# Performance work log

Measured on AMD Instinct MI355X. Metric: run time of the kernel, lower is better.

## Reference

```python
import jax, jax.numpy as jnp
import numpy as np
import math

KEY_SIZE = 128  # init arg; scale = 1/sqrt(key_size)


def setup_inputs() -> dict:
    key = jax.random.key(0)
    kq, kk, kv = jax.random.split(key, 3)
    B, LQ, LK, D, DV = 16, 2048, 2048, 128, 128
    q = jax.random.normal(kq, (B, LQ, D), dtype=jnp.float32)
    k = jax.random.normal(kk, (B, LK, D), dtype=jnp.float32)
    v = jax.random.normal(kv, (B, LK, DV), dtype=jnp.float32)
    return {"q": q, "k": k, "v": v}


def reference(q, k, v):
    scale = 1.0 / math.sqrt(KEY_SIZE)
    # scores: [B, Lq, Lk]
    scores = jnp.einsum('bqd,bkd->bqk', q, k) * scale
    probs = jax.nn.softmax(scores, axis=-1)
    # dropout with p=0.0 is identity (eval-equivalent)
    return jnp.einsum('bqk,bkv->bqv', probs, v)
```

## Files before the change

### kernel.cpp

```cpp
#include <hip/hip_runtime.h>
#include <hip/hip_bf16.h>

typedef float f32x4 __attribute__((ext_vector_type(4)));
typedef float f32x16 __attribute__((ext_vector_type(16)));
typedef short bf16x8 __attribute__((ext_vector_type(8)));
typedef unsigned u32x4 __attribute__((ext_vector_type(4)));

constexpr int NB = 16, LQ = 2048, LK = 2048, D = 128, DV = 128;
constexpr int NTH = 32;
constexpr float SCALE = 0.08838834764831843f;
constexpr float LOG2E = 1.4426950408889634f;
constexpr float QSCALE = SCALE * LOG2E;
constexpr float SHIFT = 12.0f;

__device__ __forceinline__ unsigned short f2bfs(float f) {
  __hip_bfloat16 h = __float2bfloat16(f);
  return __builtin_bit_cast(unsigned short, h);
}

__device__ __forceinline__ unsigned short f2bf(float f) {
  unsigned int u = __float_as_uint(f);
  u += 0x7FFFu + ((u >> 16) & 1u);
  return (unsigned short)(u >> 16);
}

__device__ __forceinline__ int swz2(int row) {
  return (row ^ (row >> 1) ^ (row >> 3)) & 7;
}

__device__ __forceinline__ int swap23(int m) {
  return (m & ~12) | ((m & 4) << 1) | ((m & 8) >> 1);
}

typedef const __attribute__((address_space(1))) void* gas1_t;
typedef __attribute__((address_space(3))) void* las3_t;
__device__ __forceinline__ void gload16(const void* g, void* l) {
  __builtin_amdgcn_global_load_lds((gas1_t)g, (las3_t)l, 16, 0, 0);
}

__device__ __forceinline__ unsigned pk2(float lo, float hi) {
  unsigned short a = f2bfs(lo), b = f2bfs(hi);
  return (unsigned)a | ((unsigned)b << 16);
}

__device__ __forceinline__ void mk_pb(const f32x16& s, bf16x8& pe, bf16x8& po) {
  u32x4 e = {pk2(s[0], s[1]), pk2(s[2], s[3]), pk2(s[4], s[5]), pk2(s[6], s[7])};
  pe = __builtin_bit_cast(bf16x8, e);
  u32x4 od = {pk2(s[8], s[9]), pk2(s[10], s[11]), pk2(s[12], s[13]), pk2(s[14], s[15])};
  po = __builtin_bit_cast(bf16x8, od);
}

__global__ __launch_bounds__(256) void conv_k2(const float* __restrict__ kp,
                                               unsigned short* __restrict__ out) {
  __shared__ __align__(16) unsigned short tk[4096];
  const int T = blockIdx.x, b = blockIdx.y;
  const int tid = threadIdx.x;
  const int k = tid >> 3, cc = tid & 7, d0 = cc * 16;
  const float* src = kp + ((long)(b * LK) + 32 * T + k) * D + d0;
  f32x4 a0 = ((const f32x4*)src)[0];
  f32x4 a1 = ((const f32x4*)src)[1];
  f32x4 a2 = ((const f32x4*)src)[2];
  f32x4 a3 = ((const f32x4*)src)[3];
  bf16x8 r0, r1;
  #pragma unroll
  for (int j = 0; j < 4; ++j) {
    r0[j] = (short)f2bfs(a0[j]); r0[4 + j] = (short)f2bfs(a1[j]);
    r1[j] = (short)f2bfs(a2[j]); r1[4 + j] = (short)f2bfs(a3[j]);
  }
  const int rr = swap23(k);
  *(bf16x8*)&tk[(2 * cc) * 256 + rr * 8] = r0;
  *(bf16x8*)&tk[(2 * cc + 1) * 256 + rr * 8] = r1;
  __syncthreads();
  unsigned short* dst = out + ((long)(b * 64 + T)) * 4096 + tid * 16;
  *(bf16x8*)dst = *(const bf16x8*)&tk[tid * 16];
  *(bf16x8*)(dst + 8) = *(const bf16x8*)&tk[tid * 16 + 8];
}

__global__ __launch_bounds__(256) void conv_v2(const float* __restrict__ vp,
                                               unsigned short* __restrict__ out) {
  __shared__ __align__(16) unsigned short tv[4096];
  const int T = blockIdx.x, b = blockIdx.y;
  const int tid = threadIdx.x;
  const int k = tid >> 3, cc = tid & 7, d0 = cc * 16;
  const float* src = vp + ((long)(b * LK) + 32 * T + k) * DV + d0;
  f32x4 a0 = ((const f32x4*)src)[0];
  f32x4 a1 = ((const f32x4*)src)[1];
  f32x4 a2 = ((const f32x4*)src)[2];
  f32x4 a3 = ((const f32x4*)src)[3];
  unsigned short vals[16];
  #pragma unroll
  for (int j = 0; j < 4; ++j) {
    vals[j]      = f2bfs(a0[j]);
    vals[4 + j]  = f2bfs(a1[j]);
    vals[8 + j]  = f2bfs(a2[j]);
    vals[12 + j] = f2bfs(a3[j]);
  }
  const int vbase = (k >> 3) * 1024 + (k & 7);
  #pragma unroll
  for (int i = 0; i < 16; ++i)
    tv[vbase + (d0 + i) * 8] = vals[i];
  __syncthreads();
  unsigned short* dst = out + ((long)(b * 64 + T)) * 4096 + tid * 16;
  *(bf16x8*)dst = *(const bf16x8*)&tv[tid * 16];
  *(bf16x8*)(dst + 8) = *(const bf16x8*)&tv[tid * 16 + 8];
}

__global__ __launch_bounds__(128, 2) void attn_fwd13(
    const float* __restrict__ qp, const unsigned short* __restrict__ wsK2,
    const unsigned short* __restrict__ wsV2, float* __restrict__ op) {
  __shared__ __align__(16) unsigned short sm[16384];

  const int tid = threadIdx.x;
  const int wid = tid >> 6;
  const int lane = tid & 63;
  const int q32 = lane & 31;
  const int hi  = lane >> 5;

  const int bid = blockIdx.x;
  const int sbid = (bid & 7) * 128 + (bid >> 3);
  const int b = sbid >> 6;
  const int qb = (sbid & 63) * 32;

  bf16x8 aq[8];
  {
    const float* qrow = qp + ((long)(b * LQ + qb + q32)) * D + hi * 8;
    #pragma unroll
    for (int st = 0; st < 8; ++st) {
      f32x4 x0 = *(const f32x4*)(qrow + st * 16);
      f32x4 x1 = *(const f32x4*)(qrow + st * 16 + 4);
      #pragma unroll
      for (int j = 0; j < 4; ++j) {
        aq[st][j]     = (short)f2bfs(x0[j] * QSCALE);
        aq[st][4 + j] = (short)f2bfs(x1[j] * QSCALE);
      }
    }
  }
  __builtin_amdgcn_sched_barrier(0);

  const int lbase = wid * 8192;
  const unsigned short* kps = wsK2 + ((long)(b * 64 + wid * 32)) * 4096;
  const unsigned short* vgb = wsV2 + ((long)(b * 64 + wid * 32)) * 4096
                              + hi * 1024 + q32 * 8;

  auto stageK = [&](int buf, int t) {
    const long toff = (long)t * 4096;
    const int lb = lbase + buf * 4096;
    #pragma unroll
    for (int it = 0; it < 8; ++it) {
      const int ci = it * 64 + lane;
      gload16(kps + toff + ci * 8, &sm[lb + ci * 8]);
    }
  };

  stageK(0, 0);
  stageK(1, 1);

  f32x16 o[4];
  #pragma unroll
  for (int mt = 0; mt < 4; ++mt) o[mt] = (f32x16){};
  float l_s = 0.f;

  const int kub = lbase + hi * 256 + q32 * 8;

  f32x16 sA, sB;
  bf16x8 vfA[8], vfB[8];

  asm volatile("s_waitcnt vmcnt(8)" ::: "memory");
  __builtin_amdgcn_sched_barrier(0);
  #pragma unroll
  for (int i = 0; i < 16; ++i) sA[i] = -SHIFT;
  #pragma unroll
  for (int st = 0; st < 8; ++st) {
    bf16x8 k0 = *(const bf16x8*)&sm[kub + st * 512];
    sA = __builtin_amdgcn_mfma_f32_32x32x16_bf16(k0, aq[st], sA, 0, 0, 0);
  }
  #pragma unroll
  for (int ks = 0; ks < 2; ++ks)
    #pragma unroll
    for (int mt = 0; mt < 4; ++mt)
      vfA[ks * 4 + mt] = *(const bf16x8*)(vgb + ks * 2048 + mt * 256);
  asm volatile("s_waitcnt lgkmcnt(0)" ::: "memory");
  __builtin_amdgcn_sched_barrier(0);
  stageK(0, 2);

  auto body = [&](int t, f32x16& s_prev, f32x16& s_next,
                  bf16x8 (&v_prev)[8], bf16x8 (&v_next)[8]) {
    if (t < NTH - 1) {
      asm volatile("s_waitcnt vmcnt(8)" ::: "memory");
    } else {
      asm volatile("s_waitcnt vmcnt(0)" ::: "memory");
    }
    __builtin_amdgcn_sched_barrier(0);

    const int kb = kub + (t & 1) * 4096;

    #pragma unroll
    for (int i = 0; i < 16; ++i) s_next[i] = -SHIFT;
    __builtin_amdgcn_s_setprio(1);
    #pragma unroll
    for (int st = 0; st < 8; ++st) {
      bf16x8 k0 = *(const bf16x8*)&sm[kb + st * 512];
      s_next = __builtin_amdgcn_mfma_f32_32x32x16_bf16(k0, aq[st], s_next, 0, 0, 0);
    }
    __builtin_amdgcn_s_setprio(0);

    const unsigned short* vt = vgb + (long)t * 4096;
    #pragma unroll
    for (int ks = 0; ks < 2; ++ks)
      #pragma unroll
      for (int mt = 0; mt < 4; ++mt)
        v_next[ks * 4 + mt] = *(const bf16x8*)(vt + ks * 2048 + mt * 256);

    #pragma unroll
    for (int i = 0; i < 16; ++i) s_prev[i] = exp2f(s_prev[i]);
    float s8[8];
    #pragma unroll
    for (int i = 0; i < 8; ++i) s8[i] = s_prev[i] + s_prev[i + 8];
    float sum = ((s8[0] + s8[1]) + (s8[2] + s8[3])) +
                ((s8[4] + s8[5]) + (s8[6] + s8[7]));
    l_s += sum + __shfl_xor(sum, 32);
    bf16x8 pb0, pb1;
    mk_pb(s_prev, pb0, pb1);

    __builtin_amdgcn_s_setprio(1);
    #pragma unroll
    for (int mt = 0; mt < 4; ++mt)
      o[mt] = __builtin_amdgcn_mfma_f32_32x32x16_bf16(v_prev[mt], pb0, o[mt], 0, 0, 0);
    #pragma unroll
    for (int mt = 0; mt < 4; ++mt)
      o[mt] = __builtin_amdgcn_mfma_f32_32x32x16_bf16(v_prev[4 + mt], pb1, o[mt], 0, 0, 0);
    __builtin_amdgcn_s_setprio(0);

    asm volatile("s_waitcnt lgkmcnt(0)" ::: "memory");
    __builtin_amdgcn_sched_barrier(0);
    if (t + 2 < NTH) stageK(t & 1, t + 2);
  };

  for (int tt = 1; tt < NTH - 1; tt += 2) {
    body(tt,     sA, sB, vfA, vfB);
    body(tt + 1, sB, sA, vfB, vfA);
  }
  body(NTH - 1, sA, sB, vfA, vfB);

  {
    asm volatile("s_waitcnt vmcnt(0)" ::: "memory");
    __builtin_amdgcn_sched_barrier(0);
    #pragma unroll
    for (int i = 0; i < 16; ++i) sB[i] = exp2f(sB[i]);
    float s8[8];
    #pragma unroll
    for (int i = 0; i < 8; ++i) s8[i] = sB[i] + sB[i + 8];
    float sum = ((s8[0] + s8[1]) + (s8[2] + s8[3])) +
                ((s8[4] + s8[5]) + (s8[6] + s8[7]));
    l_s += sum + __shfl_xor(sum, 32);
    bf16x8 pb0, pb1;
    mk_pb(sB, pb0, pb1);
    #pragma unroll
    for (int mt = 0; mt < 4; ++mt)
      o[mt] = __builtin_amdgcn_mfma_f32_32x32x16_bf16(vfB[mt], pb0, o[mt], 0, 0, 0);
    #pragma unroll
    for (int mt = 0; mt < 4; ++mt)
      o[mt] = __builtin_amdgcn_mfma_f32_32x32x16_bf16(vfB[4 + mt], pb1, o[mt], 0, 0, 0);
  }

  float* wreg = (float*)sm;
  __syncthreads();
  if (wid == 1) {
    #pragma unroll
    for (int j4 = 0; j4 < 16; ++j4) {
      const int mt = j4 >> 2, a = j4 & 3;
      f32x4 v = {o[mt][4 * a], o[mt][4 * a + 1], o[mt][4 * a + 2], o[mt][4 * a + 3]};
      *(f32x4*)&wreg[lane * 64 + ((j4 ^ (lane & 15)) << 2)] = v;
    }
    wreg[4096 + lane] = l_s;
  }
  __syncthreads();
  if (wid == 0) {
    const float l1 = wreg[4096 + lane];
    const float inv = 1.f / (l_s + l1);
    float* dst = op + ((long)(b * LQ + qb + q32)) * DV;
    #pragma unroll
    for (int j4 = 0; j4 < 16; ++j4) {
      const int mt = j4 >> 2, a = j4 & 3;
      f32x4 pv = *(const f32x4*)&wreg[lane * 64 + ((j4 ^ (lane & 15)) << 2)];
      f32x4 r;
      #pragma unroll
      for (int i = 0; i < 4; ++i) r[i] = (o[mt][4 * a + i] + pv[i]) * inv;
      *(f32x4*)&dst[32 * mt + 8 * a + 4 * hi] = r;
    }
  }
}

__device__ __forceinline__ int swzc(int row, int c16) {
  return c16 ^ ((row ^ (row >> 3)) & 7);
}

__global__ __launch_bounds__(256, 2) void attn_fwd(
    const float* __restrict__ qp, const float* __restrict__ kp,
    const float* __restrict__ vp, float* __restrict__ op) {
  __shared__ __align__(16) unsigned short smm[28672];
  const int tid = threadIdx.x, wid = tid >> 6, lane = tid & 63;
  const int g = lane >> 4, c = lane & 15;
  const int b = blockIdx.y, qb = blockIdx.x * 64;
  const float* qg = qp + ((long)b * LQ + qb) * D;
  const float* kg = kp + (long)b * LK * D;
  const float* vg = vp + (long)b * LK * DV;
  #pragma unroll
  for (int it = 0; it < 4; ++it) {
    int ch = it * 256 + tid, row = ch >> 4, c16 = ch & 15;
    const float* src = qg + row * D + c16 * 8;
    f32x4 f0 = *(const f32x4*)(src);
    f32x4 f1 = *(const f32x4*)(src + 4);
    bf16x8 fr;
    #pragma unroll
    for (int j = 0; j < 4; ++j) {
      fr[j] = (short)f2bf(f0[j] * SCALE);
      fr[4 + j] = (short)f2bf(f1[j] * SCALE);
    }
    *(bf16x8*)&smm[row * 128 + swzc(row, c16) * 8] = fr;
  }
  __syncthreads();
  bf16x8 aq[4];
  #pragma unroll
  for (int ks = 0; ks < 4; ++ks) {
    int row = wid * 16 + c;
    aq[ks] = *(const bf16x8*)&smm[row * 128 + swzc(row, ks * 4 + g) * 8];
  }
  f32x4 o[8]; f32x4 fz = {0.f, 0.f, 0.f, 0.f};
  #pragma unroll
  for (int i = 0; i < 8; ++i) o[i] = fz;
  float m_r[4] = {-1e30f, -1e30f, -1e30f, -1e30f};
  float l_r[4] = {0.f, 0.f, 0.f, 0.f};
  const int pbase = 24576 + wid * 1024;
  for (int kv0 = 0; kv0 < LK; kv0 += 64) {
    __syncthreads();
    const float* ksrc = kg + (long)kv0 * D;
    #pragma unroll
    for (int it = 0; it < 4; ++it) {
      int ch = it * 256 + tid, row = ch >> 4, c16 = ch & 15;
      const float* src = ksrc + row * D + c16 * 8;
      f32x4 f0 = *(const f32x4*)(src);
      f32x4 f1 = *(const f32x4*)(src + 4);
      bf16x8 fr;
      #pragma unroll
      for (int j = 0; j < 4; ++j) { fr[j] = (short)f2bf(f0[j]); fr[4 + j] = (short)f2bf(f1[j]); }
      *(bf16x8*)&smm[8192 + row * 128 + swzc(row, c16) * 8] = fr;
    }
    {
      const float* vsrc = vg + (long)kv0 * DV;
      int dvq = (tid & 31) * 4, kg8 = tid >> 5;
      f32x4 col[8];
      #pragma unroll
      for (int j = 0; j < 8; ++j) col[j] = *(const f32x4*)(vsrc + (kg8 * 8 + j) * DV + dvq);
      #pragma unroll
      for (int i = 0; i < 4; ++i) {
        int dv = dvq + i;
        bf16x8 fr;
        #pragma unroll
        for (int j = 0; j < 8; ++j) fr[j] = (short)f2bf(col[j][i]);
        *(bf16x8*)&smm[16384 + dv * 64 + swzc(dv, kg8) * 8] = fr;
      }
    }
    __syncthreads();
    f32x4 s[4];
    #pragma unroll
    for (int i = 0; i < 4; ++i) s[i] = fz;
    #pragma unroll
    for (int ks = 0; ks < 4; ++ks) {
      #pragma unroll
      for (int t = 0; t < 4; ++t) {
        int row = t * 16 + c;
        bf16x8 bk = *(const bf16x8*)&smm[8192 + row * 128 + swzc(row, ks * 4 + g) * 8];
        s[t] = __builtin_amdgcn_mfma_f32_16x16x32_bf16(aq[ks], bk, s[t], 0, 0, 0);
      }
    }
    #pragma unroll
    for (int r = 0; r < 4; ++r) {
      float pm = fmaxf(fmaxf(s[0][r], s[1][r]), fmaxf(s[2][r], s[3][r]));
      pm = fmaxf(pm, __shfl_xor(pm, 1));
      pm = fmaxf(pm, __shfl_xor(pm, 2));
      pm = fmaxf(pm, __shfl_xor(pm, 4));
      pm = fmaxf(pm, __shfl_xor(pm, 8));
      float mn = fmaxf(m_r[r], pm);
      float al = exp2f((m_r[r] - mn) * LOG2E);
      float sum = 0.f;
      #pragma unroll
      for (int t = 0; t < 4; ++t) {
        float p = exp2f((s[t][r] - mn) * LOG2E);
        s[t][r] = p; sum += p;
      }
      sum += __shfl_xor(sum, 1); sum += __shfl_xor(sum, 2);
      sum += __shfl_xor(sum, 4); sum += __shfl_xor(sum, 8);
      l_r[r] = l_r[r] * al + sum; m_r[r] = mn;
      #pragma unroll
      for (int dvt = 0; dvt < 8; ++dvt) o[dvt][r] *= al;
    }
    #pragma unroll
    for (int t = 0; t < 4; ++t)
      #pragma unroll
      for (int r = 0; r < 4; ++r) {
        int row = g * 4 + r, colx = c + 16 * t;
        smm[pbase + row * 64 + swzc(row, colx >> 3) * 8 + (colx & 7)] = f2bf(s[t][r]);
      }
    #pragma unroll
    for (int ks = 0; ks < 2; ++ks) {
      bf16x8 pa = *(const bf16x8*)&smm[pbase + c * 64 + swzc(c, ks * 4 + g) * 8];
      #pragma unroll
      for (int dvt = 0; dvt < 8; ++dvt) {
        int row = dvt * 16 + c;
        bf16x8 vb2 = *(const bf16x8*)&smm[16384 + row * 64 + swzc(row, ks * 4 + g) * 8];
        o[dvt] = __builtin_amdgcn_mfma_f32_16x16x32_bf16(pa, vb2, o[dvt], 0, 0, 0);
      }
    }
  }
  float* dst = op + ((long)b * LQ + qb + wid * 16) * DV;
  #pragma unroll
  for (int r = 0; r < 4; ++r) {
    float inv = 1.f / l_r[r];
    #pragma unroll
    for (int dvt = 0; dvt < 8; ++dvt)
      dst[(g * 4 + r) * DV + dvt * 16 + c] = o[dvt][r] * inv;
  }
}

extern "C" void kernel_launch(void* const* d_in, const int* in_sizes, int n_in,
                              void* d_out, int out_size, void* d_ws, size_t ws_size,
                              hipStream_t stream) {
  const float* q = (const float*)d_in[0];
  const float* k = (const float*)d_in[1];
  const float* v = (const float*)d_in[2];
  float* out = (float*)d_out;

  const size_t kelems = (size_t)NB * LK * D;
  const size_t need = kelems * 2 * 2;
  if (ws_size >= need) {
    unsigned short* wsK2 = (unsigned short*)d_ws;
    unsigned short* wsV2 = wsK2 + kelems;
    conv_k2<<<dim3(LK / 32, NB), dim3(256), 0, stream>>>(k, wsK2);
    conv_v2<<<dim3(LK / 32, NB), dim3(256), 0, stream>>>(v, wsV2);
    attn_fwd13<<<dim3(NB * LQ / 32), dim3(128), 0, stream>>>(q, wsK2, wsV2, out);
  } else {
    attn_fwd<<<dim3(LQ / 64, NB), dim3(256), 0, stream>>>(q, k, v, out);
  }
}
```

Before: 74.21 us.

## Split key range across four waves with single-buffered K and tree reduction

The attention kernel now runs 4 waves per 32-query block instead of 2, each wave handling 16 key tiles instead of 32, with launch bounds raised to 256 threads and 3 blocks per CU. K staging drops from double to single buffering in LDS, and V fragments move to a single register set loaded after the PV MFMAs. The final merge becomes a two-level LDS reduction across four waves with extra barriers. The aim is more parallelism and latency hiding per CU, at the cost of less intra-wave prefetch overlap and a longer epilogue.

```diff
diff --git a/kernel.cpp b/kernel.cpp
--- a/kernel.cpp
+++ b/kernel.cpp
@@ -7,7 +7,7 @@
 typedef unsigned u32x4 __attribute__((ext_vector_type(4)));
 
 constexpr int NB = 16, LQ = 2048, LK = 2048, D = 128, DV = 128;
-constexpr int NTH = 32;
+constexpr int NT = 16;
 constexpr float SCALE = 0.08838834764831843f;
 constexpr float LOG2E = 1.4426950408889634f;
 constexpr float QSCALE = SCALE * LOG2E;
@@ -105,10 +105,10 @@
   *(bf16x8*)(dst + 8) = *(const bf16x8*)&tv[tid * 16 + 8];
 }
 
-__global__ __launch_bounds__(128, 2) void attn_fwd13(
+__global__ __launch_bounds__(256, 3) void attn_fwd15(
     const float* __restrict__ qp, const unsigned short* __restrict__ wsK2,
     const unsigned short* __restrict__ wsV2, float* __restrict__ op) {
-  __shared__ __align__(16) unsigned short sm[16384];
+  __shared__ __align__(16) unsigned short sm[17408];
 
   const int tid = threadIdx.x;
   const int wid = tid >> 6;
@@ -137,23 +137,19 @@
   }
   __builtin_amdgcn_sched_barrier(0);
 
-  const int lbase = wid * 8192;
-  const unsigned short* kps = wsK2 + ((long)(b * 64 + wid * 32)) * 4096;
-  const unsigned short* vgb = wsV2 + ((long)(b * 64 + wid * 32)) * 4096
+  const int lbase = wid * 4096;
+  const unsigned short* kps = wsK2 + ((long)(b * 64 + wid * 16)) * 4096;
+  const unsigned short* vgb = wsV2 + ((long)(b * 64 + wid * 16)) * 4096
                               + hi * 1024 + q32 * 8;
 
-  auto stageK = [&](int buf, int t) {
+  auto stageK = [&](int t) {
     const long toff = (long)t * 4096;
-    const int lb = lbase + buf * 4096;
     #pragma unroll
     for (int it = 0; it < 8; ++it) {
       const int ci = it * 64 + lane;
-      gload16(kps + toff + ci * 8, &sm[lb + ci * 8]);
+      gload16(kps + toff + ci * 8, &sm[lbase + ci * 8]);
     }
   };
-
-  stageK(0, 0);
-  stageK(1, 1);
 
   f32x16 o[4];
   #pragma unroll
@@ -163,9 +159,10 @@
   const int kub = lbase + hi * 256 + q32 * 8;
 
   f32x16 sA, sB;
-  bf16x8 vfA[8], vfB[8];
-
-  asm volatile("s_waitcnt vmcnt(8)" ::: "memory");
+  bf16x8 vf[8];
+
+  stageK(0);
+  asm volatile("s_waitcnt vmcnt(0)" ::: "memory");
   __builtin_amdgcn_sched_barrier(0);
   #pragma unroll
   for (int i = 0; i < 16; ++i) sA[i] = -SHIFT;
@@ -174,42 +171,38 @@
     bf16x8 k0 = *(const bf16x8*)&sm[kub + st * 512];
     sA = __builtin_amdgcn_mfma_f32_32x32x16_bf16(k0, aq[st], sA, 0, 0, 0);
   }
-  #pragma unroll
-  for (int ks = 0; ks < 2; ++ks)
-    #pragma unroll
-    for (int mt = 0; mt < 4; ++mt)
-      vfA[ks * 4 + mt] = *(const bf16x8*)(vgb + ks * 2048 + mt * 256);
   asm volatile("s_waitcnt lgkmcnt(0)" ::: "memory");
   __builtin_amdgcn_sched_barrier(0);
-  stageK(0, 2);
-
-  auto body = [&](int t, f32x16& s_prev, f32x16& s_next,
-                  bf16x8 (&v_prev)[8], bf16x8 (&v_next)[8]) {
-    if (t < NTH - 1) {
+  stageK(1);
+  #pragma unroll
+  for (int ks = 0; ks < 2; ++ks)
+    #pragma unroll
+    for (int mt = 0; mt < 4; ++mt)
+      vf[ks * 4 + mt] = *(const bf16x8*)(vgb + ks * 2048 + mt * 256);
+
+  auto body = [&](int t, f32x16& s_prev, f32x16& s_next) {
+    asm volatile("s_waitcnt vmcnt(8)" ::: "memory");
+    __builtin_amdgcn_sched_barrier(0);
+
+    #pragma unroll
+    for (int i = 0; i < 16; ++i) s_next[i] = -SHIFT;
+    __builtin_amdgcn_s_setprio(1);
+    #pragma unroll
+    for (int st = 0; st < 8; ++st) {
+      bf16x8 k0 = *(const bf16x8*)&sm[kub + st * 512];
+      s_next = __builtin_amdgcn_mfma_f32_32x32x16_bf16(k0, aq[st], s_next, 0, 0, 0);
+    }
+    __builtin_amdgcn_s_setprio(0);
+
+    asm volatile("s_waitcnt lgkmcnt(0)" ::: "memory");
+    __builtin_amdgcn_sched_barrier(0);
+    if (t + 1 < NT) {
+      stageK(t + 1);
       asm volatile("s_waitcnt vmcnt(8)" ::: "memory");
     } else {
       asm volatile("s_waitcnt vmcnt(0)" ::: "memory");
     }
     __builtin_amdgcn_sched_barrier(0);
-
-    const int kb = kub + (t & 1) * 4096;
-
-    #pragma unroll
-    for (int i = 0; i < 16; ++i) s_next[i] = -SHIFT;
-    __builtin_amdgcn_s_setprio(1);
-    #pragma unroll
-    for (int st = 0; st < 8; ++st) {
-      bf16x8 k0 = *(const bf16x8*)&sm[kb + st * 512];
-      s_next = __builtin_amdgcn_mfma_f32_32x32x16_bf16(k0, aq[st], s_next, 0, 0, 0);
-    }
-    __builtin_amdgcn_s_setprio(0);
-
-    const unsigned short* vt = vgb + (long)t * 4096;
-    #pragma unroll
-    for (int ks = 0; ks < 2; ++ks)
-      #pragma unroll
-      for (int mt = 0; mt < 4; ++mt)
-        v_next[ks * 4 + mt] = *(const bf16x8*)(vt + ks * 2048 + mt * 256);
 
     #pragma unroll
     for (int i = 0; i < 16; ++i) s_prev[i] = exp2f(s_prev[i]);
@@ -225,22 +218,25 @@
     __builtin_amdgcn_s_setprio(1);
     #pragma unroll
     for (int mt = 0; mt < 4; ++mt)
-      o[mt] = __builtin_amdgcn_mfma_f32_32x32x16_bf16(v_prev[mt], pb0, o[mt], 0, 0, 0);
+      o[mt] = __builtin_amdgcn_mfma_f32_32x32x16_bf16(vf[mt], pb0, o[mt], 0, 0, 0);
     #pragma unroll
     for (int mt = 0; mt < 4; ++mt)
-      o[mt] = __builtin_amdgcn_mfma_f32_32x32x16_bf16(v_prev[4 + mt], pb1, o[mt], 0, 0, 0);
+      o[mt] = __builtin_amdgcn_mfma_f32_32x32x16_bf16(vf[4 + mt], pb1, o[mt], 0, 0, 0);
     __builtin_amdgcn_s_setprio(0);
 
-    asm volatile("s_waitcnt lgkmcnt(0)" ::: "memory");
-    __builtin_amdgcn_sched_barrier(0);
-    if (t + 2 < NTH) stageK(t & 1, t + 2);
+    const unsigned short* vt = vgb + (long)t * 4096;
+    #pragma unroll
+    for (int ks = 0; ks < 2; ++ks)
+      #pragma unroll
+      for (int mt = 0; mt < 4; ++mt)
+        vf[ks * 4 + mt] = *(const bf16x8*)(vt + ks * 2048 + mt * 256);
   };
 
-  for (int tt = 1; tt < NTH - 1; tt += 2) {
-    body(tt,     sA, sB, vfA, vfB);
-    body(tt + 1, sB, sA, vfB, vfA);
-  }
-  body(NTH - 1, sA, sB, vfA, vfB);
+  for (int tt = 1; tt + 1 < NT; tt += 2) {
+    body(tt,     sA, sB);
+    body(tt + 1, sB, sA);
+  }
+  body(NT - 1, sA, sB);
 
   {
     asm volatile("s_waitcnt vmcnt(0)" ::: "memory");
@@ -257,35 +253,55 @@
     mk_pb(sB, pb0, pb1);
     #pragma unroll
     for (int mt = 0; mt < 4; ++mt)
-      o[mt] = __builtin_amdgcn_mfma_f32_32x32x16_bf16(vfB[mt], pb0, o[mt], 0, 0, 0);
+      o[mt] = __builtin_amdgcn_mfma_f32_32x32x16_bf16(vf[mt], pb0, o[mt], 0, 0, 0);
     #pragma unroll
     for (int mt = 0; mt < 4; ++mt)
-      o[mt] = __builtin_amdgcn_mfma_f32_32x32x16_bf16(vfB[4 + mt], pb1, o[mt], 0, 0, 0);
-  }
-
-  float* wreg = (float*)sm;
-  __syncthreads();
-  if (wid == 1) {
+      o[mt] = __builtin_amdgcn_mfma_f32_32x32x16_bf16(vf[4 + mt], pb1, o[mt], 0, 0, 0);
+  }
+
+  float* scr = (float*)sm;
+  float* rgA = scr;
+  float* rgB = scr + 4160;
+
+  auto wr_region = [&](float* rg) {
     #pragma unroll
     for (int j4 = 0; j4 < 16; ++j4) {
       const int mt = j4 >> 2, a = j4 & 3;
       f32x4 v = {o[mt][4 * a], o[mt][4 * a + 1], o[mt][4 * a + 2], o[mt][4 * a + 3]};
-      *(f32x4*)&wreg[lane * 64 + ((j4 ^ (lane & 15)) << 2)] = v;
-    }
-    wreg[4096 + lane] = l_s;
-  }
-  __syncthreads();
-  if (wid == 0) {
-    const float l1 = wreg[4096 + lane];
-    const float inv = 1.f / (l_s + l1);
-    float* dst = op + ((long)(b * LQ + qb + q32)) * DV;
+      *(f32x4*)&rg[lane * 64 + ((j4 ^ (lane & 15)) << 2)] = v;
+    }
+    rg[4096 + lane] = l_s;
+  };
+  auto add_region = [&](const float* rg) {
     #pragma unroll
     for (int j4 = 0; j4 < 16; ++j4) {
       const int mt = j4 >> 2, a = j4 & 3;
-      f32x4 pv = *(const f32x4*)&wreg[lane * 64 + ((j4 ^ (lane & 15)) << 2)];
+      f32x4 pv = *(const f32x4*)&rg[lane * 64 + ((j4 ^ (lane & 15)) << 2)];
+      #pragma unroll
+      for (int i = 0; i < 4; ++i) o[mt][4 * a + i] += pv[i];
+    }
+    l_s += rg[4096 + lane];
+  };
+
+  __syncthreads();
+  if (wid == 1) wr_region(rgA);
+  if (wid == 3) wr_region(rgB);
+  __syncthreads();
+  if (wid == 0) add_region(rgA);
+  if (wid == 2) add_region(rgB);
+  __syncthreads();
+  if (wid == 2) wr_region(rgA);
+  __syncthreads();
+  if (wid == 0) {
+    add_region(rgA);
+    const float inv = 1.f / l_s;
+    float* dst = op + ((long)(b * LQ + qb + q32)) * DV;
+    #pragma unroll
+    for (int j4 = 0; j4 < 16; ++j4) {
+      const int mt = j4 >> 2, a = j4 & 3;
       f32x4 r;
       #pragma unroll
-      for (int i = 0; i < 4; ++i) r[i] = (o[mt][4 * a + i] + pv[i]) * inv;
+      for (int i = 0; i < 4; ++i) r[i] = o[mt][4 * a + i] * inv;
       *(f32x4*)&dst[32 * mt + 8 * a + 4 * hi] = r;
     }
   }
@@ -438,7 +454,7 @@
     unsigned short* wsV2 = wsK2 + kelems;
     conv_k2<<<dim3(LK / 32, NB), dim3(256), 0, stream>>>(k, wsK2);
     conv_v2<<<dim3(LK / 32, NB), dim3(256), 0, stream>>>(v, wsV2);
-    attn_fwd13<<<dim3(NB * LQ / 32), dim3(128), 0, stream>>>(q, wsK2, wsV2, out);
+    attn_fwd15<<<dim3(NB * LQ / 32), dim3(256), 0, stream>>>(q, wsK2, wsV2, out);
   } else {
     attn_fwd<<<dim3(LQ / 64, NB), dim3(256), 0, stream>>>(q, k, v, out);
   }
```

After: 209.5 us. +182.3%, slower.
